# Optimization experiments

Hardware: AMD Instinct MI355X
Metric: run time of the kernel (lower is better)

The kernel has to match this reference:

```python
import jax, jax.numpy as jnp
import numpy as np
from jax import lax

DG = 8  # deformable groups


def conv3(x, w, b):
    # 3x3 stride-1 SAME conv, NCHW/OIHW
    y = lax.conv_general_dilated(x, w, (1, 1), 'SAME',
                                 dimension_numbers=('NCHW', 'OIHW', 'NCHW'))
    return y + b[None, :, None, None]


def lrelu(x):
    return jnp.where(x >= 0, x, 0.1 * x)


def _mdcn(x, offset, mask, w, b, dg):
    """Modulated deformable conv v2: 3x3, stride 1, pad 1, dilation 1, groups 1.
    offset: [B, 2*dg*9, H, W] (first dg*9 = y offsets, second dg*9 = x offsets),
    mask:   [B, dg*9, H, W] (already sigmoided)."""
    B, C, H, W = x.shape
    kk = 9
    Cg = C // dg
    off = offset.reshape(B, 2, dg, kk, H, W)
    oy, ox = off[:, 0], off[:, 1]            # [B, dg, kk, H, W]
    m = mask.reshape(B, dg, kk, H, W)
    ky = (jnp.arange(kk) // 3 - 1).astype(x.dtype).reshape(1, 1, kk, 1, 1)
    kx = (jnp.arange(kk) % 3 - 1).astype(x.dtype).reshape(1, 1, kk, 1, 1)
    hg = jnp.arange(H, dtype=x.dtype).reshape(1, 1, 1, H, 1)
    wg = jnp.arange(W, dtype=x.dtype).reshape(1, 1, 1, 1, W)
    py = hg + ky + oy                        # sampling positions (pad=1 cancels k-1 shift)
    px = wg + kx + ox
    y0 = jnp.floor(py)
    x0 = jnp.floor(px)
    wy = py - y0
    wx = px - x0
    xg = x.reshape(B, dg, Cg, H * W)
    acc = jnp.zeros((B, dg, Cg, kk, H, W), x.dtype)
    for dy, dx, wgt in ((0.0, 0.0, (1 - wy) * (1 - wx)),
                        (0.0, 1.0, (1 - wy) * wx),
                        (1.0, 0.0, wy * (1 - wx)),
                        (1.0, 1.0, wy * wx)):
        yy = y0 + dy
        xx = x0 + dx
        valid = (yy >= 0) & (yy < H) & (xx >= 0) & (xx < W)
        yi = jnp.clip(yy, 0, H - 1).astype(jnp.int32)
        xi = jnp.clip(xx, 0, W - 1).astype(jnp.int32)
        idx = (yi * W + xi).reshape(B, dg, 1, kk * H * W)
        v = jnp.take_along_axis(xg, idx, axis=3).reshape(B, dg, Cg, kk, H, W)
        acc = acc + v * (wgt * valid.astype(x.dtype))[:, :, None]
    acc = acc * m[:, :, None]                # modulation mask
    sampled = acc.reshape(B, C, kk, H, W)
    out = jnp.einsum('bckhw,ock->bohw', sampled, w.reshape(w.shape[0], C, kk))
    return out + b[None, :, None, None]


def _dcn_pack(x, feat, w_om, b_om, w, b):
    out = conv3(feat, w_om, b_om)            # [B, 3*dg*9, H, W]
    o1, o2, mr = jnp.split(out, 3, axis=1)
    offset = jnp.concatenate([o1, o2], axis=1)
    mask = jax.nn.sigmoid(mr)
    return _mdcn(x, offset, mask, w, b, DG)


def _forward(ref, neb,
             w_oc1, b_oc1, w_om1, b_om1, w_dcn1, b_dcn1, w_fc, b_fc,
             w_cas1, b_cas1, w_cas2, b_cas2, w_om2, b_om2, w_dcn2, b_dcn2,
             w_ta1, b_ta1, w_ta2, b_ta2, w_ff, b_ff):
    start = ref
    # --- PCD alignment (nbr_feat_l = neb, ref_feat_l = ref) ---
    off = lrelu(conv3(jnp.concatenate([neb, ref], axis=1), w_oc1, b_oc1))
    feat = _dcn_pack(neb, off, w_om1, b_om1, w_dcn1, b_dcn1)
    feat = lrelu(conv3(feat, w_fc, b_fc))
    off = jnp.concatenate([feat, ref], axis=1)
    off = lrelu(conv3(lrelu(conv3(off, w_cas1, b_cas1)), w_cas2, b_cas2))
    feat = lrelu(_dcn_pack(feat, off, w_om2, b_om2, w_dcn2, b_dcn2))
    # --- TSA fusion (ref=ref, neb=feat) ---
    emb_ref = conv3(ref, w_ta1, b_ta1)
    emb = conv3(feat, w_ta2, b_ta2)
    corr = jnp.sum(emb * emb_ref, axis=1, keepdims=True)  # [B,1,H,W]
    feat = lrelu(conv3(ref * corr, w_ff, b_ff))
    return feat + start


def setup_inputs() -> dict:
    key = jax.random.key(0)
    ks = jax.random.split(key, 32)
    B, C, H, W = 4, 64, 180, 320
    s = 0.05
    p = lambda k, shape: (jax.random.normal(k, shape, jnp.float32) * s)
    OM = 3 * DG * 9  # 216
    return {
        'ref': jax.random.normal(ks[0], (B, C, H, W), jnp.float32),
        'neb': jax.random.normal(ks[1], (B, C, H, W), jnp.float32),
        'w_oc1': p(ks[2], (C, 2 * C, 3, 3)), 'b_oc1': p(ks[3], (C,)),
        'w_om1': p(ks[4], (OM, C, 3, 3)),    'b_om1': p(ks[5], (OM,)),
        'w_dcn1': p(ks[6], (C, C, 3, 3)),    'b_dcn1': p(ks[7], (C,)),
        'w_fc': p(ks[8], (C, C, 3, 3)),      'b_fc': p(ks[9], (C,)),
        'w_cas1': p(ks[10], (C, 2 * C, 3, 3)), 'b_cas1': p(ks[11], (C,)),
        'w_cas2': p(ks[12], (C, C, 3, 3)),   'b_cas2': p(ks[13], (C,)),
        'w_om2': p(ks[14], (OM, C, 3, 3)),   'b_om2': p(ks[15], (OM,)),
        'w_dcn2': p(ks[16], (C, C, 3, 3)),   'b_dcn2': p(ks[17], (C,)),
        'w_ta1': p(ks[18], (C, C, 3, 3)),    'b_ta1': p(ks[19], (C,)),
        'w_ta2': p(ks[20], (C, C, 3, 3)),    'b_ta2': p(ks[21], (C,)),
        'w_ff': p(ks[22], (C, C, 3, 3)),     'b_ff': p(ks[23], (C,)),
    }


def reference(ref, neb,
              w_oc1, b_oc1, w_om1, b_om1, w_dcn1, b_dcn1, w_fc, b_fc,
              w_cas1, b_cas1, w_cas2, b_cas2, w_om2, b_om2, w_dcn2, b_dcn2,
              w_ta1, b_ta1, w_ta2, b_ta2, w_ff, b_ff):
    return _forward(ref, neb,
                    w_oc1, b_oc1, w_om1, b_om1, w_dcn1, b_dcn1, w_fc, b_fc,
                    w_cas1, b_cas1, w_cas2, b_cas2, w_om2, b_om2, w_dcn2, b_dcn2,
                    w_ta1, b_ta1, w_ta2, b_ta2, w_ff, b_ff)
```

## Files before the change

kernel.cpp:

```cpp
#include <hip/hip_runtime.h>
#include <cmath>


using short8 = __attribute__((ext_vector_type(8))) short;
using f32x4  = __attribute__((ext_vector_type(4))) float;
using f32x2  = __attribute__((ext_vector_type(2))) float;

#define DEVINL static __device__ __forceinline__

DEVINL unsigned short f2bf(float f){
    unsigned u = __float_as_uint(f);
    u += 0x7fffu + ((u >> 16) & 1u);
    return (unsigned short)(u >> 16);
}
DEVINL unsigned pack2(float a, float b){ return (unsigned)f2bf(a) | ((unsigned)f2bf(b) << 16); }
DEVINL float bflo(unsigned u){ return __uint_as_float(u << 16); }
DEVINL float bfhi(unsigned u){ return __uint_as_float(u & 0xffff0000u); }
DEVINL float bf2f(unsigned short u){ return __uint_as_float((unsigned)u << 16); }
DEVINL float lrelu_f(float v){ return v >= 0.f ? v : 0.1f * v; }
DEVINL f32x2 up2(unsigned u){
    return f32x2{__uint_as_float(u << 16), __uint_as_float(u & 0xffff0000u)};
}

DEVINL void swz_decode(int& bx, int& by, int& bz){
    const int gx = gridDim.x, gy = gridDim.y;
    int lin = blockIdx.x + gx * (blockIdx.y + gy * blockIdx.z);
    int nwg = gx * gy * gridDim.z;
    int q = nwg >> 3, r = nwg & 7;
    int xcd = lin & 7, idx = lin >> 3;
    int swz = (xcd < r ? xcd * (q + 1) : r + xcd * q) + idx;
    bz = swz / (gx * gy);
    int rem = swz - bz * gx * gy;
    by = rem / gx; bx = rem - by * gx;
}

struct Ptr4 { unsigned short* p[4]; };

__global__ __launch_bounds__(256) void nchw2nhwc2(const float* __restrict__ inA,
                                                  const float* __restrict__ inB,
                                                  unsigned short* __restrict__ outA,
                                                  unsigned short* __restrict__ outB)
{
    constexpr int HW = 180 * 320;
    const int blk = blockIdx.x;
    const float* in = (blk < 900) ? inA : inB;
    unsigned short* out = (blk < 900) ? outA : outB;
    size_t idx = (size_t)(blk % 900) * 256 + threadIdx.x;
    size_t bb = idx / HW, p = idx % HW;
    const float* src = in + (bb * 64) * (size_t)HW + p;
    unsigned short* dst = out + idx * 64;
    #pragma unroll
    for (int c0 = 0; c0 < 64; c0 += 16) {
        unsigned r[8];
        #pragma unroll
        for (int q = 0; q < 8; ++q)
            r[q] = pack2(src[(size_t)(c0 + 2*q) * HW], src[(size_t)(c0 + 2*q + 1) * HW]);
        *(uint4*)(dst + c0)     = *(uint4*)&r[0];
        *(uint4*)(dst + c0 + 8) = *(uint4*)&r[4];
    }
}

struct PrepArgs {
    const float* src[11];
    unsigned short* dst[11];
    int cout[11]; int cin[11]; int nch[11]; int kind[11];
};

__global__ __launch_bounds__(256) void prep_all(PrepArgs a)
{
    const int t = blockIdx.y;
    const int idx = blockIdx.x * 256 + threadIdx.x;
    if (a.kind[t] == 1) {
        if (idx >= 36864) return;
        int kk = idx & 31, oc = (idx >> 5) & 63, s = idx >> 11;
        int k = s * 32 + kk;
        int gt = k >> 3, c8 = k & 7;
        int g = gt / 9, tp = gt - g * 9;
        a.dst[t][idx] = f2bf(a.src[t][((size_t)oc * 64 + g * 8 + c8) * 9 + tp]);
    } else {
        int cin = a.cin[t], cout = a.cout[t];
        int ncs = cin / 32;
        int total = a.nch[t] * 9 * ncs * 2048;
        if (idx >= total) return;
        int kk = idx & 31, oc_l = (idx >> 5) & 63, rest = idx >> 11;
        int cs = rest % ncs; int rest2 = rest / ncs;
        int j = rest2 % 9; int ch = rest2 / 9;
        int oc = ch * 64 + oc_l, c = cs * 32 + kk;
        float v = (oc < cout) ? a.src[t][((size_t)oc * cin + c) * 9 + j] : 0.f;
        a.dst[t][idx] = f2bf(v);
    }
}

template<bool ACT, bool SCALE, int OUTMODE, int NM, int HALVES, int TH>
__global__ __launch_bounds__(256, (TH == 2 ? 4 : 3)) void conv_mfma(
    const unsigned short* __restrict__ in0, const unsigned short* __restrict__ in1,
    const unsigned short* __restrict__ wgt, const float* __restrict__ bias,
    unsigned short* __restrict__ out, const float* __restrict__ corr,
    const float* __restrict__ res, float* __restrict__ outf,
    Ptr4 omout, int choff, int zdiv)
{
    constexpr int H = 180, W = 320, HW = H * W;
    constexpr int XW = 66;
    constexpr int HR = TH + 2;
    constexpr int NE = HR * XW * 8;
    constexpr int NFW = (TH == 4) ? 4 : 2;
    __shared__ __align__(16) unsigned char lds[HR * XW * 64 * 2];

    const int tid = threadIdx.x;
    int bx, by, bz;
    swz_decode(bx, by, bz);
    int b, ch;
    if (OUTMODE == 1) { b = bz / zdiv; ch = bz % zdiv + choff; }
    else              { b = bz; ch = 0; }
    const int x0 = bx * 64, y0 = by * TH;

    const int wv = tid >> 6, lane = tid & 63;
    const int ll = lane & 15, lh = lane >> 4;
    const int row_w = (TH == 4) ? wv : (wv & 1);
    const int nf0   = (TH == 4) ? 0  : ((wv >> 1) * 2);
    const unsigned short* wchunk = wgt + (size_t)ch * (9 * 2 * 2048);
    const int alane = ll * 32 + lh * 8;

    f32x4 acc[NM][NFW];
    #pragma unroll
    for (int mi = 0; mi < NM; ++mi)
        #pragma unroll
        for (int nf = 0; nf < NFW; ++nf) acc[mi][nf] = f32x4{0.f, 0.f, 0.f, 0.f};

    #pragma unroll
    for (int h = 0; h < HALVES; ++h) {
        if (h) __syncthreads();
        const unsigned short* srcb = (HALVES == 2 && h == 1) ? in1 : in0;
        for (int t = tid; t < NE; t += 256) {
            int cb = t & 7; int r = t >> 3;
            int xp = r % XW, yp = r / XW;
            int gx = x0 - 1 + xp, gy = y0 - 1 + yp;
            uint4 v = make_uint4(0, 0, 0, 0);
            if (gx >= 0 && gx < W && gy >= 0 && gy < H) {
                size_t pix = (size_t)b * HW + (size_t)gy * W + gx;
                v = *(const uint4*)(srcb + pix * 64 + cb * 8);
                if (SCALE) {
                    float cv = corr[pix];
                    v.x = pack2(bflo(v.x) * cv, bfhi(v.x) * cv);
                    v.y = pack2(bflo(v.y) * cv, bfhi(v.y) * cv);
                    v.z = pack2(bflo(v.z) * cv, bfhi(v.z) * cv);
                    v.w = pack2(bflo(v.w) * cv, bfhi(v.w) * cv);
                }
            }
            int blk = cb ^ (xp & 7);
            *(uint4*)&lds[(size_t)((yp * XW + xp) * 8 + blk) * 16] = v;
        }
        __syncthreads();

        #pragma unroll
        for (int j = 0; j < 9; ++j) {
            const int jy = j / 3, jx = j % 3;
            #pragma unroll
            for (int csl = 0; csl < 2; ++csl) {
                const int ws = j * (2 * HALVES) + h * 2 + csl;
                short8 a[NM];
                #pragma unroll
                for (int mi = 0; mi < NM; ++mi)
                    a[mi] = *(const short8*)(wchunk + (size_t)ws * 2048 + mi * 512 + alane);
                short8 bf[NFW];
                #pragma unroll
                for (int nfl = 0; nfl < NFW; ++nfl) {
                    int xp = (nf0 + nfl) * 16 + ll + jx;
                    int blk = (csl * 4 + lh) ^ (xp & 7);
                    int addr = (((row_w + jy) * XW + xp) * 8 + blk) * 16;
                    bf[nfl] = *(const short8*)&lds[addr];
                }
                #pragma unroll
                for (int mi = 0; mi < NM; ++mi)
                    #pragma unroll
                    for (int nfl = 0; nfl < NFW; ++nfl)
                        acc[mi][nfl] = __builtin_amdgcn_mfma_f32_16x16x32_bf16(a[mi], bf[nfl], acc[mi][nfl], 0, 0, 0);
            }
        }
    }

    const int py = y0 + row_w;
    const size_t pixrow = (size_t)b * HW + (size_t)py * W;

    if (OUTMODE == 1) {
        if constexpr (TH == 4) {
            __syncthreads();
            unsigned short* t2 = (unsigned short*)lds;
            #pragma unroll
            for (int nfl = 0; nfl < NFW; ++nfl) {
                const int px = nfl * 16 + ll;
                #pragma unroll
                for (int mi = 0; mi < NM; ++mi) {
                    #pragma unroll
                    for (int jj = 0; jj < 4; ++jj) {
                        int oc = mi * 16 + lh * 4 + jj;
                        int ocg = ch * 64 + oc;
                        if (ocg < 216) {
                            float t = acc[mi][nfl][jj] + bias[ocg];
                            t2[(size_t)(wv * 64 + oc) * 72 + px] = f2bf(ACT ? lrelu_f(t) : t);
                        }
                    }
                }
            }
            __syncthreads();
            unsigned short* oslot = omout.p[b];
            #pragma unroll
            for (int i = 0; i < 8; ++i) {
                int gu = i * 32 + (tid >> 3), q = tid & 7;
                int row = gu >> 6, oc = gu & 63;
                int ocg = ch * 64 + oc;
                if (oc < NM * 16 && ocg < 216) {
                    uint4 v = *(uint4*)&t2[(size_t)(row * 64 + oc) * 72 + q * 8];
                    *(uint4*)&oslot[(size_t)ocg * HW + (size_t)(y0 + row) * W + x0 + q * 8] = v;
                }
            }
        }
        return;
    }

    #pragma unroll
    for (int nfl = 0; nfl < NFW; ++nfl) {
        const int px = x0 + (nf0 + nfl) * 16 + ll;
        #pragma unroll
        for (int mi = 0; mi < NM; ++mi) {
            const int oc_l = mi * 16 + lh * 4;
            if (OUTMODE == 0) {
                float v[4];
                #pragma unroll
                for (int jj = 0; jj < 4; ++jj) {
                    float t = acc[mi][nfl][jj] + bias[oc_l + jj];
                    v[jj] = ACT ? lrelu_f(t) : t;
                }
                uint2 st; st.x = pack2(v[0], v[1]); st.y = pack2(v[2], v[3]);
                *(uint2*)&out[(pixrow + px) * 64 + oc_l] = st;
            } else {
                #pragma unroll
                for (int jj = 0; jj < 4; ++jj) {
                    int oc = oc_l + jj;
                    float t = acc[mi][nfl][jj] + bias[oc];
                    if (ACT) t = lrelu_f(t);
                    size_t idx = ((size_t)b * 64 + oc) * HW + (size_t)py * W + px;
                    outf[idx] = t + res[idx];
                }
            }
        }
    }
}

__global__ __launch_bounds__(256, 3) void tacorr_mfma(
    const unsigned short* __restrict__ inR,
    const unsigned short* __restrict__ inE,
    const unsigned short* __restrict__ wR, const float* __restrict__ bR,
    const unsigned short* __restrict__ wE, const float* __restrict__ bE,
    float* __restrict__ outf)
{
    constexpr int H = 180, W = 320, HW = H * W;
    constexpr int NE1 = 6 * 34 * 8;
    __shared__ __align__(16) unsigned char lds[2][6 * 34 * 64 * 2];

    const int tid = threadIdx.x;
    int bx, by, bz;
    swz_decode(bx, by, bz);
    const int b = bz;
    const int x0 = bx * 32, y0 = by * 4;

    for (int t = tid; t < 2 * NE1; t += 256) {
        int half = t / NE1, e = t - half * NE1;
        int cb = e & 7; int r = e >> 3;
        int xp = r % 34, yp = r / 34;
        int gx = x0 - 1 + xp, gy = y0 - 1 + yp;
        uint4 v = make_uint4(0, 0, 0, 0);
        if (gx >= 0 && gx < W && gy >= 0 && gy < H) {
            size_t pix = (size_t)b * HW + (size_t)gy * W + gx;
            const unsigned short* src = (half ? inE : inR) + pix * 64 + cb * 8;
            v = *(const uint4*)src;
        }
        int blk = cb ^ (xp & 7);
        *(uint4*)&lds[half][(size_t)((yp * 34 + xp) * 8 + blk) * 16] = v;
    }
    __syncthreads();

    const int wv = tid >> 6, lane = tid & 63;
    const int ll = lane & 15, lh = lane >> 4;
    const int alane = ll * 32 + lh * 8;

    f32x4 accR[4][2], accE[4][2];
    #pragma unroll
    for (int mi = 0; mi < 4; ++mi)
        #pragma unroll
        for (int nf = 0; nf < 2; ++nf) { accR[mi][nf] = f32x4{0,0,0,0}; accE[mi][nf] = f32x4{0,0,0,0}; }

    #pragma unroll
    for (int j = 0; j < 9; ++j) {
        const int jy = j / 3, jx = j % 3;
        #pragma unroll
        for (int cs = 0; cs < 2; ++cs) {
            const int s = j * 2 + cs;
            short8 aR[4], aE[4];
            #pragma unroll
            for (int mi = 0; mi < 4; ++mi) {
                aR[mi] = *(const short8*)(wR + (size_t)s * 2048 + mi * 512 + alane);
                aE[mi] = *(const short8*)(wE + (size_t)s * 2048 + mi * 512 + alane);
            }
            #pragma unroll
            for (int nf = 0; nf < 2; ++nf) {
                int xp = nf * 16 + ll + jx;
                int blk = (cs * 4 + lh) ^ (xp & 7);
                int addr = (((wv + jy) * 34 + xp) * 8 + blk) * 16;
                short8 bfR = *(const short8*)&lds[0][addr];
                short8 bfE = *(const short8*)&lds[1][addr];
                #pragma unroll
                for (int mi = 0; mi < 4; ++mi) {
                    accR[mi][nf] = __builtin_amdgcn_mfma_f32_16x16x32_bf16(aR[mi], bfR, accR[mi][nf], 0, 0, 0);
                    accE[mi][nf] = __builtin_amdgcn_mfma_f32_16x16x32_bf16(aE[mi], bfE, accE[mi][nf], 0, 0, 0);
                }
            }
        }
    }

    const int py = y0 + wv;
    const size_t pixrow = (size_t)b * HW + (size_t)py * W;
    #pragma unroll
    for (int nf = 0; nf < 2; ++nf) {
        const int px = x0 + nf * 16 + ll;
        float dot = 0.f;
        #pragma unroll
        for (int mi = 0; mi < 4; ++mi) {
            const int oc_l = mi * 16 + lh * 4;
            #pragma unroll
            for (int jj = 0; jj < 4; ++jj)
                dot += (accR[mi][nf][jj] + bR[oc_l + jj]) * (accE[mi][nf][jj] + bE[oc_l + jj]);
        }
        dot += __shfl_xor(dot, 16);
        dot += __shfl_xor(dot, 32);
        if (lh == 0) outf[pixrow + px] = dot;
    }
}

template<int ACT>
__global__ __launch_bounds__(256, 4) void mdcn_mfma(
    const unsigned short* __restrict__ x, Ptr4 omslots,
    const unsigned short* __restrict__ wgt, const float* __restrict__ bias,
    unsigned short* __restrict__ out)
{
    constexpr int H = 180, W = 320, HW = H * W;
    constexpr size_t CHW = (size_t)HW * 64;
    __shared__ __align__(16) unsigned char sv[72 * 32 * 16];

    const int tid = threadIdx.x;
    int bx, by, bz;
    swz_decode(bx, by, bz);
    const unsigned short* xb  = x + (size_t)bz * CHW;
    const unsigned short* omb = omslots.p[bz];
    unsigned short* ob        = out + (size_t)bz * CHW;
    const int px0 = bx * 32;
    const int py  = by;

    {
        const int pxl = tid & 31, g = tid >> 5;
        const int px = px0 + pxl;
        const size_t p = (size_t)py * W + px;
        const unsigned short* omg = omb + (size_t)(g * 9) * HW + p;

        float oyv[9], oxv[9], mmv[9];
        #pragma unroll
        for (int k = 0; k < 9; ++k) oyv[k] = bf2f(omg[(size_t)k * HW]);
        #pragma unroll
        for (int k = 0; k < 9; ++k) oxv[k] = bf2f(omg[(size_t)(72 + k) * HW]);
        #pragma unroll
        for (int k = 0; k < 9; ++k) mmv[k] = bf2f(omg[(size_t)(144 + k) * HW]);

        #pragma unroll
        for (int k = 0; k < 9; ++k) {
            float m = 1.f / (1.f + __expf(-mmv[k]));
            float pyf = (float)(py + (k / 3) - 1) + oyv[k];
            float pxf = (float)(px + (k % 3) - 1) + oxv[k];
            float y0f = floorf(pyf), x0f = floorf(pxf);
            float wy = pyf - y0f, wx = pxf - x0f;
            int yi = (int)y0f, xi = (int)x0f;
            bool vy0 = (yi >= 0) && (yi < H);
            bool vy1 = (yi + 1 >= 0) && (yi + 1 < H);
            bool vx0 = (xi >= 0) && (xi < W);
            bool vx1 = (xi + 1 >= 0) && (xi + 1 < W);
            float w00 = (vy0 && vx0) ? (1.f - wy) * (1.f - wx) * m : 0.f;
            float w01 = (vy0 && vx1) ? (1.f - wy) * wx * m : 0.f;
            float w10 = (vy1 && vx0) ? wy * (1.f - wx) * m : 0.f;
            float w11 = (vy1 && vx1) ? wy * wx * m : 0.f;
            int yc0 = min(max(yi, 0), H - 1), yc1 = min(max(yi + 1, 0), H - 1);
            int xc0 = min(max(xi, 0), W - 1), xc1 = min(max(xi + 1, 0), W - 1);
            uint4 c00 = *(const uint4*)(xb + ((size_t)(yc0 * W + xc0) * 64 + g * 8));
            uint4 c01 = *(const uint4*)(xb + ((size_t)(yc0 * W + xc1) * 64 + g * 8));
            uint4 c10 = *(const uint4*)(xb + ((size_t)(yc1 * W + xc0) * 64 + g * 8));
            uint4 c11 = *(const uint4*)(xb + ((size_t)(yc1 * W + xc1) * 64 + g * 8));
            const unsigned* p00 = (const unsigned*)&c00;
            const unsigned* p01 = (const unsigned*)&c01;
            const unsigned* p10 = (const unsigned*)&c10;
            const unsigned* p11 = (const unsigned*)&c11;
            unsigned r[4];
            #pragma unroll
            for (int q = 0; q < 4; ++q) {
                f32x2 rv = up2(p00[q]) * w00 + up2(p01[q]) * w01
                         + up2(p10[q]) * w10 + up2(p11[q]) * w11;
                r[q] = pack2(rv[0], rv[1]);
            }
            *(uint4*)&sv[(size_t)((g * 9 + k) * 32 + pxl) * 16] = *(uint4*)r;
        }
    }
    __syncthreads();

    const int wv = tid >> 6, lane = tid & 63;
    const int ll = lane & 15, lh = lane >> 4;
    f32x4 acc[2] = {f32x4{0.f,0.f,0.f,0.f}, f32x4{0.f,0.f,0.f,0.f}};
    #pragma unroll
    for (int s = 0; s < 18; ++s) {
        short8 a = *(const short8*)(wgt + (size_t)(s * 64 + wv * 16 + ll) * 32 + lh * 8);
        #pragma unroll
        for (int nf = 0; nf < 2; ++nf) {
            short8 bb = *(const short8*)&sv[(size_t)s * 2048 + lh * 512 + (nf * 16 + ll) * 16];
            acc[nf] = __builtin_amdgcn_mfma_f32_16x16x32_bf16(a, bb, acc[nf], 0, 0, 0);
        }
    }
    #pragma unroll
    for (int nf = 0; nf < 2; ++nf) {
        int opx = px0 + nf * 16 + ll;
        int oc0 = wv * 16 + lh * 4;
        float v[4];
        #pragma unroll
        for (int jj = 0; jj < 4; ++jj) {
            float t = acc[nf][jj] + bias[oc0 + jj];
            v[jj] = ACT ? lrelu_f(t) : t;
        }
        uint2 st; st.x = pack2(v[0], v[1]); st.y = pack2(v[2], v[3]);
        *(uint2*)&ob[((size_t)py * W + opx) * 64 + oc0] = st;
    }
}

extern "C" void kernel_launch(void* const* d_in, const int* in_sizes, int n_in,
                              void* d_out, int out_size, void* d_ws, size_t ws_size,
                              hipStream_t stream)
{
    const float* ref    = (const float*)d_in[0];
    const float* neb    = (const float*)d_in[1];
    const float* w_oc1  = (const float*)d_in[2];  const float* b_oc1  = (const float*)d_in[3];
    const float* w_om1  = (const float*)d_in[4];  const float* b_om1  = (const float*)d_in[5];
    const float* w_dcn1 = (const float*)d_in[6];  const float* b_dcn1 = (const float*)d_in[7];
    const float* w_fc   = (const float*)d_in[8];  const float* b_fc   = (const float*)d_in[9];
    const float* w_cas1 = (const float*)d_in[10]; const float* b_cas1 = (const float*)d_in[11];
    const float* w_cas2 = (const float*)d_in[12]; const float* b_cas2 = (const float*)d_in[13];
    const float* w_om2  = (const float*)d_in[14]; const float* b_om2  = (const float*)d_in[15];
    const float* w_dcn2 = (const float*)d_in[16]; const float* b_dcn2 = (const float*)d_in[17];
    const float* w_ta1  = (const float*)d_in[18]; const float* b_ta1  = (const float*)d_in[19];
    const float* w_ta2  = (const float*)d_in[20]; const float* b_ta2  = (const float*)d_in[21];
    const float* w_ff   = (const float*)d_in[22]; const float* b_ff   = (const float*)d_in[23];

    constexpr int H = 180, W = 320, HW = H * W;
    constexpr size_t CHW = (size_t)HW * 64;
    constexpr size_t SLB = 4 * CHW * 2;
    constexpr size_t OMSLOT_EL = (size_t)HW * 216;
    constexpr size_t OMSLOT_B  = OMSLOT_EL * 2;

    char* wsb = (char*)d_ws;
    unsigned short* S0 = (unsigned short*)(wsb);
    unsigned short* S1 = (unsigned short*)(wsb + SLB);
    unsigned short* S2 = (unsigned short*)(wsb + 2 * SLB);
    unsigned short* S3 = (unsigned short*)(wsb + 3 * SLB);
    float* corrf = (float*)S3;
    unsigned short* ffw = (unsigned short*)(wsb + SLB + (2u << 20));

    char* doutb = (char*)d_out;
    unsigned short* omA0 = (unsigned short*)doutb;
    unsigned short* omA1 = omA0 + OMSLOT_EL;
    unsigned short* wb   = (unsigned short*)(doutb + 2 * OMSLOT_B);
    const bool big = ws_size >= 4 * SLB + 2 * OMSLOT_B;
    unsigned short* omB0 = (unsigned short*)(wsb + 4 * SLB);
    unsigned short* omB1 = omB0 + OMSLOT_EL;

    unsigned short* w_oc1p = wb + 0;
    unsigned short* w_om1p = wb + 73728;
    unsigned short* w_dcn1p= wb + 221184;
    unsigned short* w_fcp  = wb + 258048;
    unsigned short* w_cas1p= wb + 294912;
    unsigned short* w_cas2p= wb + 368640;
    unsigned short* w_om2p = wb + 405504;
    unsigned short* w_dcn2p= wb + 552960;
    unsigned short* w_ta1p = wb + 589824;
    unsigned short* w_ta2p = wb + 626688;
    unsigned short* w_ffp  = wb + 663552;

    dim3 blk(256);
    dim3 gf(5, 90, 4);
    dim3 g2(10, 45, 4);
    Ptr4 none{};

    nchw2nhwc2<<<1800, blk, 0, stream>>>(ref, neb, S0, S1);

    {
        PrepArgs pa;
        const float* srcs[11] = {w_oc1, w_om1, w_dcn1, w_fc, w_cas1, w_cas2, w_om2, w_dcn2, w_ta1, w_ta2, w_ff};
        unsigned short* dsts[11] = {w_oc1p, w_om1p, w_dcn1p, w_fcp, w_cas1p, w_cas2p, w_om2p, w_dcn2p, w_ta1p, w_ta2p, w_ffp};
        int couts[11] = {64, 216, 0, 64, 64, 64, 216, 0, 64, 64, 64};
        int cins[11]  = {128, 64, 0, 64, 128, 64, 64, 0, 64, 64, 64};
        int nchs[11]  = {1, 4, 0, 1, 1, 1, 4, 0, 1, 1, 1};
        int kinds[11] = {0, 0, 1, 0, 0, 0, 0, 1, 0, 0, 0};
        for (int i = 0; i < 11; ++i) {
            pa.src[i] = srcs[i]; pa.dst[i] = dsts[i];
            pa.cout[i] = couts[i]; pa.cin[i] = cins[i]; pa.nch[i] = nchs[i]; pa.kind[i] = kinds[i];
        }
        prep_all<<<dim3(576, 11), blk, 0, stream>>>(pa);
    }

    conv_mfma<true, false, 0, 4, 2, 2><<<gf, blk, 0, stream>>>(
        S1, S0, w_oc1p, b_oc1, S2, nullptr, nullptr, nullptr, none, 0, 1);

    auto ompack = [&](const unsigned short* inp, const unsigned short* wp, const float* bp,
                      Ptr4 slots, int nb){
        conv_mfma<false, false, 1, 4, 1, 4><<<dim3(5, 45, 3 * nb), blk, 0, stream>>>(
            inp, nullptr, wp, bp, nullptr, nullptr, nullptr, nullptr, slots, 0, 3);
        conv_mfma<false, false, 1, 2, 1, 4><<<dim3(5, 45, nb), blk, 0, stream>>>(
            inp, nullptr, wp, bp, nullptr, nullptr, nullptr, nullptr, slots, 3, 1);
    };

    if (big) {
        Ptr4 slots{omA0, omA1, omB0, omB1};
        ompack(S2, w_om1p, b_om1, slots, 4);
        mdcn_mfma<0><<<dim3(10, 180, 4), blk, 0, stream>>>(S1, slots, w_dcn1p, b_dcn1, S3);
    } else {
        Ptr4 slots{omA0, omA1, nullptr, nullptr};
        for (int pp = 0; pp < 2; ++pp) {
            ompack(S2 + 2 * pp * CHW, w_om1p, b_om1, slots, 2);
            mdcn_mfma<0><<<dim3(10, 180, 2), blk, 0, stream>>>(S1 + 2 * pp * CHW, slots,
                                                               w_dcn1p, b_dcn1, S3 + 2 * pp * CHW);
        }
    }

    conv_mfma<true, false, 0, 4, 1, 2><<<gf, blk, 0, stream>>>(
        S3, nullptr, w_fcp, b_fc, S2, nullptr, nullptr, nullptr, none, 0, 1);
    conv_mfma<true, false, 0, 4, 2, 2><<<gf, blk, 0, stream>>>(
        S2, S0, w_cas1p, b_cas1, S1, nullptr, nullptr, nullptr, none, 0, 1);
    conv_mfma<true, false, 0, 4, 1, 2><<<gf, blk, 0, stream>>>(
        S1, nullptr, w_cas2p, b_cas2, S3, nullptr, nullptr, nullptr, none, 0, 1);

    if (big) {
        Ptr4 slots{omA0, omA1, omB0, omB1};
        ompack(S3, w_om2p, b_om2, slots, 4);
        mdcn_mfma<1><<<dim3(10, 180, 4), blk, 0, stream>>>(S2, slots, w_dcn2p, b_dcn2, S1);
    } else {
        Ptr4 slots{omA0, omA1, nullptr, nullptr};
        for (int pp = 0; pp < 2; ++pp) {
            ompack(S3 + 2 * pp * CHW, w_om2p, b_om2, slots, 2);
            mdcn_mfma<1><<<dim3(10, 180, 2), blk, 0, stream>>>(S2 + 2 * pp * CHW, slots,
                                                               w_dcn2p, b_dcn2, S1 + 2 * pp * CHW);
        }
    }

    tacorr_mfma<<<g2, blk, 0, stream>>>(S0, S1, w_ta1p, b_ta1, w_ta2p, b_ta2, corrf);

    hipMemcpyAsync(ffw, w_ffp, 36864 * 2, hipMemcpyDeviceToDevice, stream);

    conv_mfma<true, true, 2, 4, 1, 2><<<gf, blk, 0, stream>>>(
        S0, nullptr, ffw, b_ff, nullptr, corrf, ref, (float*)d_out, none, 0, 1);
}
```

Baseline: 1.106 ms.

## Shrink tacorr tile to two rows and merge offset-mask conv launches

The temporal-attention correlation kernel now covers a 2x32 pixel tile per block instead of 4x32. Each wave handles one row and one 16-pixel column half, which halves the accumulator registers and raises the launch bound to 4 blocks per CU, at the cost of more halo reloads and twice as many blocks. Separately, the offset/mask conv is now a single launch covering all 4 channel chunks with the 4-wide tile template, replacing the 3+1 split whose last chunk used the 2-wide variant. That last chunk may be partially padded work, since the offset/mask conv has 216 output channels.

```diff
diff --git a/kernel.cpp b/kernel.cpp
--- a/kernel.cpp
+++ b/kernel.cpp
@@ -247,7 +247,7 @@
     }
 }
 
-__global__ __launch_bounds__(256, 3) void tacorr_mfma(
+__global__ __launch_bounds__(256, 4) void tacorr_mfma(
     const unsigned short* __restrict__ inR,
     const unsigned short* __restrict__ inE,
     const unsigned short* __restrict__ wR, const float* __restrict__ bR,
@@ -255,14 +255,14 @@
     float* __restrict__ outf)
 {
     constexpr int H = 180, W = 320, HW = H * W;
-    constexpr int NE1 = 6 * 34 * 8;
-    __shared__ __align__(16) unsigned char lds[2][6 * 34 * 64 * 2];
+    constexpr int NE1 = 4 * 34 * 8;
+    __shared__ __align__(16) unsigned char lds[2][4 * 34 * 64 * 2];
 
     const int tid = threadIdx.x;
     int bx, by, bz;
     swz_decode(bx, by, bz);
     const int b = bz;
-    const int x0 = bx * 32, y0 = by * 4;
+    const int x0 = bx * 32, y0 = by * 2;
 
     for (int t = tid; t < 2 * NE1; t += 256) {
         int half = t / NE1, e = t - half * NE1;
@@ -282,13 +282,12 @@
 
     const int wv = tid >> 6, lane = tid & 63;
     const int ll = lane & 15, lh = lane >> 4;
+    const int row_w = wv & 1, nfw = wv >> 1;
     const int alane = ll * 32 + lh * 8;
 
-    f32x4 accR[4][2], accE[4][2];
-    #pragma unroll
-    for (int mi = 0; mi < 4; ++mi)
-        #pragma unroll
-        for (int nf = 0; nf < 2; ++nf) { accR[mi][nf] = f32x4{0,0,0,0}; accE[mi][nf] = f32x4{0,0,0,0}; }
+    f32x4 accR[4], accE[4];
+    #pragma unroll
+    for (int mi = 0; mi < 4; ++mi) { accR[mi] = f32x4{0,0,0,0}; accE[mi] = f32x4{0,0,0,0}; }
 
     #pragma unroll
     for (int j = 0; j < 9; ++j) {
@@ -302,39 +301,33 @@
                 aR[mi] = *(const short8*)(wR + (size_t)s * 2048 + mi * 512 + alane);
                 aE[mi] = *(const short8*)(wE + (size_t)s * 2048 + mi * 512 + alane);
             }
+            int xp = nfw * 16 + ll + jx;
+            int blk = (cs * 4 + lh) ^ (xp & 7);
+            int addr = (((row_w + jy) * 34 + xp) * 8 + blk) * 16;
+            short8 bfR = *(const short8*)&lds[0][addr];
+            short8 bfE = *(const short8*)&lds[1][addr];
             #pragma unroll
-            for (int nf = 0; nf < 2; ++nf) {
-                int xp = nf * 16 + ll + jx;
-                int blk = (cs * 4 + lh) ^ (xp & 7);
-                int addr = (((wv + jy) * 34 + xp) * 8 + blk) * 16;
-                short8 bfR = *(const short8*)&lds[0][addr];
-                short8 bfE = *(const short8*)&lds[1][addr];
-                #pragma unroll
-                for (int mi = 0; mi < 4; ++mi) {
-                    accR[mi][nf] = __builtin_amdgcn_mfma_f32_16x16x32_bf16(aR[mi], bfR, accR[mi][nf], 0, 0, 0);
-                    accE[mi][nf] = __builtin_amdgcn_mfma_f32_16x16x32_bf16(aE[mi], bfE, accE[mi][nf], 0, 0, 0);
-                }
-            }
-        }
-    }
-
-    const int py = y0 + wv;
+            for (int mi = 0; mi < 4; ++mi) {
+                accR[mi] = __builtin_amdgcn_mfma_f32_16x16x32_bf16(aR[mi], bfR, accR[mi], 0, 0, 0);
+                accE[mi] = __builtin_amdgcn_mfma_f32_16x16x32_bf16(aE[mi], bfE, accE[mi], 0, 0, 0);
+            }
+        }
+    }
+
+    const int py = y0 + row_w;
     const size_t pixrow = (size_t)b * HW + (size_t)py * W;
-    #pragma unroll
-    for (int nf = 0; nf < 2; ++nf) {
-        const int px = x0 + nf * 16 + ll;
-        float dot = 0.f;
-        #pragma unroll
-        for (int mi = 0; mi < 4; ++mi) {
-            const int oc_l = mi * 16 + lh * 4;
-            #pragma unroll
-            for (int jj = 0; jj < 4; ++jj)
-                dot += (accR[mi][nf][jj] + bR[oc_l + jj]) * (accE[mi][nf][jj] + bE[oc_l + jj]);
-        }
-        dot += __shfl_xor(dot, 16);
-        dot += __shfl_xor(dot, 32);
-        if (lh == 0) outf[pixrow + px] = dot;
-    }
+    const int px = x0 + nfw * 16 + ll;
+    float dot = 0.f;
+    #pragma unroll
+    for (int mi = 0; mi < 4; ++mi) {
+        const int oc_l = mi * 16 + lh * 4;
+        #pragma unroll
+        for (int jj = 0; jj < 4; ++jj)
+            dot += (accR[mi][jj] + bR[oc_l + jj]) * (accE[mi][jj] + bE[oc_l + jj]);
+    }
+    dot += __shfl_xor(dot, 16);
+    dot += __shfl_xor(dot, 32);
+    if (lh == 0) outf[pixrow + px] = dot;
 }
 
 template<int ACT>
@@ -489,7 +482,7 @@
 
     dim3 blk(256);
     dim3 gf(5, 90, 4);
-    dim3 g2(10, 45, 4);
+    dim3 gt(10, 90, 4);
     Ptr4 none{};
 
     nchw2nhwc2<<<1800, blk, 0, stream>>>(ref, neb, S0, S1);
@@ -514,10 +507,8 @@
 
     auto ompack = [&](const unsigned short* inp, const unsigned short* wp, const float* bp,
                       Ptr4 slots, int nb){
-        conv_mfma<false, false, 1, 4, 1, 4><<<dim3(5, 45, 3 * nb), blk, 0, stream>>>(
-            inp, nullptr, wp, bp, nullptr, nullptr, nullptr, nullptr, slots, 0, 3);
-        conv_mfma<false, false, 1, 2, 1, 4><<<dim3(5, 45, nb), blk, 0, stream>>>(
-            inp, nullptr, wp, bp, nullptr, nullptr, nullptr, nullptr, slots, 3, 1);
+        conv_mfma<false, false, 1, 4, 1, 4><<<dim3(5, 45, 4 * nb), blk, 0, stream>>>(
+            inp, nullptr, wp, bp, nullptr, nullptr, nullptr, nullptr, slots, 0, 4);
     };
 
     if (big) {
@@ -553,7 +544,7 @@
         }
     }
 
-    tacorr_mfma<<<g2, blk, 0, stream>>>(S0, S1, w_ta1p, b_ta1, w_ta2p, b_ta2, corrf);
+    tacorr_mfma<<<gt, blk, 0, stream>>>(S0, S1, w_ta1p, b_ta1, w_ta2p, b_ta2, corrf);
 
     hipMemcpyAsync(ffw, w_ffp, 36864 * 2, hipMemcpyDeviceToDevice, stream);
 
```

After: 1.138 ms. 1.03x slower.
